# Kernel optimization log

Hardware: AMD Instinct MI355X
Metric: run time of the kernel (lower is better)

Reference implementation:

```python
import jax, jax.numpy as jnp
import numpy as np

B, S, E = 2, 2048, 1024
HID = 1024
HEADS = 16
EPS = 1e-5
SCALE = (E * 2) ** (-0.5)  # source uses input_data_dim*2


def setup_inputs() -> dict:
    key = jax.random.key(0)
    k1, k2, k3 = jax.random.split(key, 3)
    return {
        "x": jax.random.normal(k1, (B, S, E), dtype=jnp.float32),
        "ln_g": jnp.ones((E,), jnp.float32),
        "ln_b": jnp.zeros((E,), jnp.float32),
        "W1": jax.random.normal(k2, (E, 3 * HID), jnp.float32) * 0.02,
        "b1": jnp.zeros((3 * HID,), jnp.float32),
        "W2": jax.random.normal(k3, (HID, HID), jnp.float32) * 0.02,
        "b2": jnp.zeros((HID,), jnp.float32),
    }


def reference(x, ln_g, ln_b, W1, b1, W2, b2):
    # LayerNorm over last dim
    mu = jnp.mean(x, axis=-1, keepdims=True)
    var = jnp.mean(jnp.square(x - mu), axis=-1, keepdims=True)
    xn = (x - mu) * jax.lax.rsqrt(var + EPS) * ln_g + ln_b
    # QKV projection: [B,S,3*HID]
    qkv = jnp.einsum('bse,ef->bsf', xn, W1) + b1
    # Faithful to source: flat reshape to (heads, B, S, 3*HID/heads)
    qkv_heads = qkv.reshape(HEADS, B, S, -1)
    q, k, v = jnp.split(qkv_heads, 3, axis=-1)  # each [H,B,S,d]
    scores = jnp.einsum('hbse,hbSe->hbsS', q, k) * SCALE  # [H,B,S,S]
    att = jax.nn.softmax(scores, axis=-1)
    full_att = jnp.einsum('hbsS,hbSe->hbse', att, v)  # [H,B,S,d]
    full_att = full_att.reshape(B, S, -1)  # faithful flat reshape -> [B,S,HID]
    out = jnp.einsum('bsh,hk->bsk', full_att, W2) + b2
    return out
```

## Files before the change

### kernel.cpp

```cpp
#include <hip/hip_runtime.h>

typedef unsigned short u16;
typedef __bf16 bf16x8 __attribute__((ext_vector_type(8)));
typedef float f32x4 __attribute__((ext_vector_type(4)));

static constexpr float SCALE2 = 0.022097086912079608f * 1.4426950408889634f;

__device__ __forceinline__ u16 f2b(float f) {
  union { float f; unsigned int i; } v; v.f = f;
  unsigned int r = v.i + 0x7fffu + ((v.i >> 16) & 1u);
  return (u16)(r >> 16);
}
__device__ __forceinline__ unsigned int pk2(float a, float b) {
#if __has_builtin(__builtin_amdgcn_cvt_pk_bf16_f32)
  auto v = __builtin_amdgcn_cvt_pk_bf16_f32(a, b);
  unsigned int u;
  __builtin_memcpy(&u, &v, 4);
  return u;
#else
  union { float f; unsigned int i; } x, y; x.f = a; y.f = b;
  return ((x.i + 0x8000u) >> 16) | ((y.i + 0x8000u) & 0xffff0000u);
#endif
}
__device__ __forceinline__ void async16(const u16* g, u16* l) {
  __builtin_amdgcn_global_load_lds((const __attribute__((address_space(1))) void*)g,
                                   (__attribute__((address_space(3))) void*)l,
                                   16, 0, 0);
}

__global__ __launch_bounds__(256) void pre_kernel(const float* __restrict__ x,
                                                  const float* __restrict__ lg,
                                                  const float* __restrict__ lb,
                                                  u16* __restrict__ xn,
                                                  const float* __restrict__ W1,
                                                  u16* __restrict__ W1T,
                                                  const float* __restrict__ W2,
                                                  u16* __restrict__ W2T) {
  __shared__ __align__(16) u16 smem[64 * 72];
  const int bx = blockIdx.x;
  const int t = threadIdx.x;
  if (bx < 4096) {
    float* red = (float*)smem;
    const int row = bx;
    float4 v = *(const float4*)(x + (size_t)row * 1024 + t * 4);
    float s = v.x + v.y + v.z + v.w;
    float ss = v.x * v.x + v.y * v.y + v.z * v.z + v.w * v.w;
    for (int off = 32; off >= 1; off >>= 1) {
      s += __shfl_xor(s, off, 64);
      ss += __shfl_xor(ss, off, 64);
    }
    const int w = t >> 6;
    if ((t & 63) == 0) { red[w] = s; red[4 + w] = ss; }
    __syncthreads();
    s = red[0] + red[1] + red[2] + red[3];
    ss = red[4] + red[5] + red[6] + red[7];
    const float mu = s * (1.0f / 1024.0f);
    const float var = ss * (1.0f / 1024.0f) - mu * mu;
    const float inv = rsqrtf(var + 1e-5f);
    float4 gg = *(const float4*)(lg + t * 4);
    float4 bb = *(const float4*)(lb + t * 4);
    ushort4 o;
    o.x = f2b((v.x - mu) * inv * gg.x + bb.x);
    o.y = f2b((v.y - mu) * inv * gg.y + bb.y);
    o.z = f2b((v.z - mu) * inv * gg.z + bb.z);
    o.w = f2b((v.w - mu) * inv * gg.w + bb.w);
    *(ushort4*)(xn + (size_t)row * 1024 + t * 4) = o;
    return;
  }
  const float* in;
  u16* out;
  int C, c0, r0;
  if (bx < 4096 + 768) {
    const int idx = bx - 4096;
    C = 3072; in = W1; out = W1T;
    c0 = (idx % 48) * 64; r0 = (idx / 48) * 64;
  } else {
    const int idx = bx - 4864;
    C = 1024; in = W2; out = W2T;
    c0 = (idx % 16) * 64; r0 = (idx / 16) * 64;
  }
  const int row = t >> 2, cseg = t & 3;
  for (int it = 0; it < 4; it++) {
    float4 v = *(const float4*)&in[(size_t)(r0 + row) * C + c0 + it * 16 + cseg * 4];
    ushort4 o;
    o.x = f2b(v.x); o.y = f2b(v.y); o.z = f2b(v.z); o.w = f2b(v.w);
    *(ushort4*)&smem[row * 72 + it * 16 + cseg * 4] = o;
  }
  __syncthreads();
  const int orow = t >> 2, ch = t & 3;
  u16 vals[16];
  for (int j = 0; j < 16; j++) vals[j] = smem[(ch * 16 + j) * 72 + orow];
  u16* dp = out + (size_t)(c0 + orow) * 1024 + r0 + ch * 16;
  *(uint4*)&dp[0] = *(uint4*)&vals[0];
  *(uint4*)&dp[8] = *(uint4*)&vals[8];
}

template <int MODE, int MT>
__global__ __launch_bounds__(256) void gemm_bt(const u16* __restrict__ A,
                                               const u16* __restrict__ Bt,
                                               const float* __restrict__ bias,
                                               float* __restrict__ C,
                                               int M, int N, int K,
                                               u16* __restrict__ Qc,
                                               u16* __restrict__ Kc,
                                               u16* __restrict__ Vtmp) {
  __shared__ __align__(16) u16 SMEM[8192];
  u16* As = SMEM;
  u16* Bs = SMEM + MT * 32;
  const int m0 = blockIdx.y * MT, n0 = blockIdx.x * 128;
  const int t = threadIdx.x, w = t >> 6, lane = t & 63;
  const int q = lane >> 4, l16 = lane & 15;
  const int wm = (w >> 1) * (MT / 2), wn = (w & 1) * 64;
  constexpr int NI = MT / 32;

  const int sc = (lane & 3) ^ ((lane >> 3) & 3);
  const u16* ap = A + (size_t)(m0 + w * 16 + (lane >> 2)) * K + sc * 8;
  const u16* bp = Bt + (size_t)(n0 + w * 16 + (lane >> 2)) * K + sc * 8;
  u16* lA = &As[w * 512];
  u16* lB = &Bs[w * 512];
  const int ac = q ^ ((l16 >> 1) & 3);

  f32x4 acc[NI][4];
  const f32x4 zero = {0.f, 0.f, 0.f, 0.f};
  for (int i = 0; i < NI; i++)
    for (int j = 0; j < 4; j++) acc[i][j] = zero;

  for (int k0 = 0; k0 < K; k0 += 32) {
    for (int i = 0; i < MT / 64; i++)
      async16(ap + (size_t)(i * 64) * K, lA + i * 2048);
    for (int i = 0; i < 2; i++)
      async16(bp + (size_t)(i * 64) * K, lB + i * 2048);
    ap += 32; bp += 32;
    __syncthreads();
    bf16x8 af[NI], bfr[4];
    for (int i = 0; i < NI; i++)
      af[i] = *(const bf16x8*)&As[(wm + i * 16 + l16) * 32 + ac * 8];
    for (int j = 0; j < 4; j++)
      bfr[j] = *(const bf16x8*)&Bs[(wn + j * 16 + l16) * 32 + ac * 8];
    for (int i = 0; i < NI; i++)
      for (int j = 0; j < 4; j++)
        acc[i][j] = __builtin_amdgcn_mfma_f32_16x16x32_bf16(af[i], bfr[j], acc[i][j], 0, 0, 0);
    __syncthreads();
  }

  if constexpr (MODE == 0) {
    for (int j = 0; j < 4; j++) {
      const int col = n0 + wn + j * 16 + l16;
      const float bv = bias[col];
      for (int i = 0; i < NI; i++) {
        const int rbase = m0 + wm + i * 16 + q * 4;
        for (int r = 0; r < 4; r++)
          C[(size_t)(rbase + r) * N + col] = acc[i][j][r] + bv;
      }
    }
  } else {
    const int seg = n0 + wn;
    const int k64 = seg >> 6;
    const int tcol = k64 / 3;
    const int typ = k64 - tcol * 3;
    u16* dst = (typ == 0) ? Qc : (typ == 1) ? Kc : Vtmp;
    const float qs = (typ == 0) ? SCALE2 : 1.0f;
    const int gidx = m0 >> 7;
    u16* tw = &SMEM[w * 1280];
    float bv[4];
    for (int j = 0; j < 4; j++) bv[j] = bias[seg + j * 16 + l16];
    __syncthreads();
    for (int i = 0; i < 4; i++) {
      for (int j = 0; j < 4; j++) {
        ushort4 pk;
        pk.x = f2b((acc[i][j][0] + bv[j]) * qs);
        pk.y = f2b((acc[i][j][1] + bv[j]) * qs);
        pk.z = f2b((acc[i][j][2] + bv[j]) * qs);
        pk.w = f2b((acc[i][j][3] + bv[j]) * qs);
        *(ushort4*)&tw[(j * 16 + l16) * 20 + q * 4] = pk;
      }
      const int r2 = lane >> 2;
      const int quarter = lane & 3;
      u16 vals[16];
      for (int c = 0; c < 16; c++)
        vals[c] = tw[(quarter * 16 + c) * 20 + r2];
      const int lr = wm + i * 16 + r2;
      const int s = (lr << 4) + tcol;
      u16* dp = dst + ((size_t)gidx * 2048 + s) * 64 + quarter * 16;
      *(uint4*)&dp[0] = *(uint4*)&vals[0];
      *(uint4*)&dp[8] = *(uint4*)&vals[8];
    }
  }
}

__global__ __launch_bounds__(256) void vtrans(const u16* __restrict__ Vtmp,
                                              u16* __restrict__ Vt) {
  __shared__ __align__(16) u16 tile[64 * 64];
  const int g = blockIdx.y, s0 = blockIdx.x * 64;
  const int t = threadIdx.x;
  const int row = t >> 3, ch = t & 7;
  for (int p = 0; p < 2; p++) {
    const int r = p * 32 + row;
    uint4 v = *(const uint4*)&Vtmp[((size_t)g * 2048 + s0 + r) * 64 + ch * 8];
    *(uint4*)&tile[r * 64 + ((ch ^ (r & 7)) * 8)] = v;
  }
  __syncthreads();
  const int d = t >> 2, scn = t & 3;
  u16 vals[16];
  for (int j2 = 0; j2 < 16; j2++) {
    const int s = scn * 16 + j2;
    vals[j2] = tile[s * 64 + (((d >> 3) ^ (s & 7)) * 8) + (d & 7)];
  }
  u16* dp = Vt + ((size_t)g * 64 + d) * 2048 + s0 + scn * 16;
  *(uint4*)&dp[0] = *(uint4*)&vals[0];
  *(uint4*)&dp[8] = *(uint4*)&vals[8];
}

__global__ __launch_bounds__(512) void attn_kernel(const u16* __restrict__ Qc,
                                                   const u16* __restrict__ Kc,
                                                   const u16* __restrict__ Vt,
                                                   u16* __restrict__ Oc) {
  __shared__ __align__(16) u16 LDS[25600];
  u16* K0 = LDS;
  u16* K1 = LDS + 4096;
  u16* V0 = LDS + 8192;
  u16* V1 = LDS + 12288;
  u16* Ps = LDS + 16384;
  const int g = blockIdx.y;
  const int q0 = blockIdx.x * 128;
  const int t = threadIdx.x, w = t >> 6, lane = t & 63;
  const int q = lane >> 4, l16 = lane & 15;

  const u16* Qg = Qc + (size_t)g * 2048 * 64;
  const u16* Kg = Kc + (size_t)g * 2048 * 64;
  const u16* Vg = Vt + (size_t)g * 64 * 2048;

  bf16x8 aq[2];
  for (int ks = 0; ks < 2; ks++)
    aq[ks] = *(const bf16x8*)&Qg[(size_t)(q0 + w * 16 + l16) * 64 + ks * 32 + q * 8];

  f32x4 accO[4];
  const f32x4 zero = {0.f, 0.f, 0.f, 0.f};
  for (int c = 0; c < 4; c++) accO[c] = zero;
  f32x4 psv = zero;

  const int ch = (lane & 7) ^ ((lane >> 3) & 7);
  const u16* kp = Kg + (size_t)(w * 8 + (lane >> 3)) * 64 + ch * 8;
  const u16* vp = Vg + (size_t)(w * 8 + (lane >> 3)) * 2048 + ch * 8;
  u16* lK0 = K0 + w * 512;
  u16* lK1 = K1 + w * 512;
  u16* lV0 = V0 + w * 512;
  u16* lV1 = V1 + w * 512;

  const int kch = q ^ (l16 & 7);
  const int pb = w * 1152;

  async16(kp, lK0);
  async16(vp, lV0);
  __syncthreads();

  for (int it = 0; it < 32; it++) {
    const int cur = it & 1;
    const u16* Kcur = cur ? K1 : K0;
    const u16* Vcur = cur ? V1 : V0;
    if (it < 31) {
      const int kt0 = (it + 1) * 64;
      async16(kp + (size_t)kt0 * 64, cur ? lK0 : lK1);
      async16(vp + kt0, cur ? lV0 : lV1);
    }

    f32x4 sa[4];
    __builtin_amdgcn_s_setprio(1);
    for (int ct = 0; ct < 4; ct++) {
      bf16x8 bk0 = *(const bf16x8*)&Kcur[(ct * 16 + l16) * 64 + kch * 8];
      bf16x8 bk1 = *(const bf16x8*)&Kcur[(ct * 16 + l16) * 64 + (kch ^ 4) * 8];
      f32x4 a = zero;
      a = __builtin_amdgcn_mfma_f32_16x16x32_bf16(bk0, aq[0], a, 0, 0, 0);
      a = __builtin_amdgcn_mfma_f32_16x16x32_bf16(bk1, aq[1], a, 0, 0, 0);
      sa[ct] = a;
    }
    __builtin_amdgcn_s_setprio(0);

    {
      u16* Pr = &Ps[pb + l16 * 72];
      for (int ct = 0; ct < 4; ct++) {
        f32x4 p;
        for (int r = 0; r < 4; r++) p[r] = __builtin_amdgcn_exp2f(sa[ct][r]);
        psv += p;
        uint2 pk;
        pk.x = pk2(p[0], p[1]);
        pk.y = pk2(p[2], p[3]);
        *(uint2*)&Pr[ct * 16 + q * 4] = pk;
      }
    }

    __builtin_amdgcn_s_setprio(1);
    for (int k2 = 0; k2 < 2; k2++) {
      bf16x8 apf = *(const bf16x8*)&Ps[pb + l16 * 72 + k2 * 32 + q * 8];
      for (int c = 0; c < 4; c++) {
        const int vch = (k2 * 4 + q) ^ (l16 & 7);
        bf16x8 bv = *(const bf16x8*)&Vcur[(c * 16 + l16) * 64 + vch * 8];
        accO[c] = __builtin_amdgcn_mfma_f32_16x16x32_bf16(bv, apf, accO[c], 0, 0, 0);
      }
    }
    __builtin_amdgcn_s_setprio(0);

    __syncthreads();
  }

  {
    float lsum = psv[0] + psv[1] + psv[2] + psv[3];
    lsum += __shfl_xor(lsum, 16, 64);
    lsum += __shfl_xor(lsum, 32, 64);
    const int srow = q0 + w * 16 + l16;
    const int orow = g * 128 + (srow >> 4);
    const int cbase = (srow & 15) * 64;
    const float linv = 1.0f / lsum;
    for (int c = 0; c < 4; c++) {
      ushort4 o;
      o.x = f2b(accO[c][0] * linv);
      o.y = f2b(accO[c][1] * linv);
      o.z = f2b(accO[c][2] * linv);
      o.w = f2b(accO[c][3] * linv);
      *(ushort4*)&Oc[(size_t)orow * 1024 + cbase + c * 16 + q * 4] = o;
    }
  }
}

extern "C" void kernel_launch(void* const* d_in, const int* in_sizes, int n_in,
                              void* d_out, int out_size, void* d_ws, size_t ws_size,
                              hipStream_t stream) {
  (void)in_sizes; (void)n_in; (void)out_size; (void)ws_size;
  const float* x    = (const float*)d_in[0];
  const float* ln_g = (const float*)d_in[1];
  const float* ln_b = (const float*)d_in[2];
  const float* W1   = (const float*)d_in[3];
  const float* b1   = (const float*)d_in[4];
  const float* W2   = (const float*)d_in[5];
  const float* b2   = (const float*)d_in[6];

  char* ws = (char*)d_ws;
  u16* xn   = (u16*)(ws);
  u16* W1T  = (u16*)(ws + ((size_t)8 << 20));
  u16* W2T  = (u16*)(ws + ((size_t)14 << 20));
  u16* Qc   = (u16*)(ws + ((size_t)16 << 20));
  u16* Kc   = (u16*)(ws + ((size_t)24 << 20));
  u16* Vtmp = (u16*)(ws + ((size_t)32 << 20));
  u16* Vt   = (u16*)(ws + ((size_t)40 << 20));
  u16* Oc   = xn;

  pre_kernel<<<dim3(5120), dim3(256), 0, stream>>>(x, ln_g, ln_b, xn, W1, W1T, W2, W2T);
  gemm_bt<1, 128><<<dim3(24, 32), dim3(256), 0, stream>>>(xn, W1T, b1, nullptr,
                                                          4096, 3072, 1024, Qc, Kc, Vtmp);
  vtrans<<<dim3(32, 32), dim3(256), 0, stream>>>(Vtmp, Vt);
  attn_kernel<<<dim3(16, 32), dim3(512), 0, stream>>>(Qc, Kc, Vt, Oc);
  gemm_bt<0, 64><<<dim3(8, 64), dim3(256), 0, stream>>>(Oc, W2T, b2, (float*)d_out,
                                                        4096, 1024, 1024, nullptr, nullptr, nullptr);
}
```

Measured before the change: 196.3 us.

## Switch attention to 32x32 MFMA with register P via permlane swap and KV split

Rewrites the attention inner loop to use 32x32x16 bf16 MFMA instructions. Each wave now handles 32 query rows and half of each 64-key tile, so eight waves cover 128 queries by splitting the KV tile in two. The softmax probabilities are repacked into MFMA operand layout in registers with permlane32_swap instead of going through an LDS scratch buffer. A final LDS reduction merges the partial O accumulators and row sums of the two KV halves. This removes the LDS round trip for P and reduces the number of MFMA issues, at the cost of an epilogue reduction, more accumulator registers and a dependence on gfx950-specific permlane instructions.

```diff
diff --git a/kernel.cpp b/kernel.cpp
--- a/kernel.cpp
+++ b/kernel.cpp
@@ -3,6 +3,9 @@
 typedef unsigned short u16;
 typedef __bf16 bf16x8 __attribute__((ext_vector_type(8)));
 typedef float f32x4 __attribute__((ext_vector_type(4)));
+typedef float f32x16 __attribute__((ext_vector_type(16)));
+typedef unsigned int u32x4 __attribute__((ext_vector_type(4)));
+typedef int i32x2 __attribute__((ext_vector_type(2)));
 
 static constexpr float SCALE2 = 0.022097086912079608f * 1.4426950408889634f;
 
@@ -20,6 +23,15 @@
 #else
   union { float f; unsigned int i; } x, y; x.f = a; y.f = b;
   return ((x.i + 0x8000u) >> 16) | ((y.i + 0x8000u) & 0xffff0000u);
+#endif
+}
+__device__ __forceinline__ i32x2 plswap(unsigned int a, unsigned int b) {
+#if __has_builtin(__builtin_amdgcn_permlane32_swap)
+  return __builtin_amdgcn_permlane32_swap((int)a, (int)b, false, false);
+#else
+  int d = (int)a, s = (int)b;
+  asm volatile("v_permlane32_swap_b32 %0, %1" : "+v"(d), "+v"(s));
+  i32x2 r; r[0] = d; r[1] = s; return r;
 #endif
 }
 __device__ __forceinline__ void async16(const u16* g, u16* l) {
@@ -220,24 +232,28 @@
   u16* K1 = LDS + 4096;
   u16* V0 = LDS + 8192;
   u16* V1 = LDS + 12288;
-  u16* Ps = LDS + 16384;
   const int g = blockIdx.y;
   const int q0 = blockIdx.x * 128;
   const int t = threadIdx.x, w = t >> 6, lane = t & 63;
-  const int q = lane >> 4, l16 = lane & 15;
+  const int l31 = lane & 31, h = lane >> 5;
+  const int qs = w & 3;
+  const int kvb = (w >> 2) * 32;
 
   const u16* Qg = Qc + (size_t)g * 2048 * 64;
   const u16* Kg = Kc + (size_t)g * 2048 * 64;
   const u16* Vg = Vt + (size_t)g * 64 * 2048;
 
-  bf16x8 aq[2];
-  for (int ks = 0; ks < 2; ks++)
-    aq[ks] = *(const bf16x8*)&Qg[(size_t)(q0 + w * 16 + l16) * 64 + ks * 32 + q * 8];
-
-  f32x4 accO[4];
-  const f32x4 zero = {0.f, 0.f, 0.f, 0.f};
-  for (int c = 0; c < 4; c++) accO[c] = zero;
-  f32x4 psv = zero;
+  bf16x8 aq[4];
+#pragma unroll
+  for (int s = 0; s < 4; s++)
+    aq[s] = *(const bf16x8*)&Qg[(size_t)(q0 + qs * 32 + l31) * 64 + s * 16 + h * 8];
+
+  f32x16 accO[2];
+#pragma unroll
+  for (int tt = 0; tt < 2; tt++)
+#pragma unroll
+    for (int r = 0; r < 16; r++) accO[tt][r] = 0.f;
+  float psv = 0.f;
 
   const int ch = (lane & 7) ^ ((lane >> 3) & 7);
   const u16* kp = Kg + (size_t)(w * 8 + (lane >> 3)) * 64 + ch * 8;
@@ -247,8 +263,7 @@
   u16* lV0 = V0 + w * 512;
   u16* lV1 = V1 + w * 512;
 
-  const int kch = q ^ (l16 & 7);
-  const int pb = w * 1152;
+  const int rsw = l31 & 7;
 
   async16(kp, lK0);
   async16(vp, lV0);
@@ -264,38 +279,42 @@
       async16(vp + kt0, cur ? lV0 : lV1);
     }
 
-    f32x4 sa[4];
+    f32x16 sa;
+#pragma unroll
+    for (int r = 0; r < 16; r++) sa[r] = 0.f;
     __builtin_amdgcn_s_setprio(1);
-    for (int ct = 0; ct < 4; ct++) {
-      bf16x8 bk0 = *(const bf16x8*)&Kcur[(ct * 16 + l16) * 64 + kch * 8];
-      bf16x8 bk1 = *(const bf16x8*)&Kcur[(ct * 16 + l16) * 64 + (kch ^ 4) * 8];
-      f32x4 a = zero;
-      a = __builtin_amdgcn_mfma_f32_16x16x32_bf16(bk0, aq[0], a, 0, 0, 0);
-      a = __builtin_amdgcn_mfma_f32_16x16x32_bf16(bk1, aq[1], a, 0, 0, 0);
-      sa[ct] = a;
+#pragma unroll
+    for (int s = 0; s < 4; s++) {
+      bf16x8 ak = *(const bf16x8*)&Kcur[(kvb + l31) * 64 + (((s * 2 + h) ^ rsw) * 8)];
+      sa = __builtin_amdgcn_mfma_f32_32x32x16_bf16(ak, aq[s], sa, 0, 0, 0);
     }
     __builtin_amdgcn_s_setprio(0);
 
-    {
-      u16* Pr = &Ps[pb + l16 * 72];
-      for (int ct = 0; ct < 4; ct++) {
-        f32x4 p;
-        for (int r = 0; r < 4; r++) p[r] = __builtin_amdgcn_exp2f(sa[ct][r]);
-        psv += p;
-        uint2 pk;
-        pk.x = pk2(p[0], p[1]);
-        pk.y = pk2(p[2], p[3]);
-        *(uint2*)&Pr[ct * 16 + q * 4] = pk;
-      }
-    }
+    float e[16];
+#pragma unroll
+    for (int r = 0; r < 16; r++) e[r] = __builtin_amdgcn_exp2f(sa[r]);
+    psv += (((e[0] + e[1]) + (e[2] + e[3])) + ((e[4] + e[5]) + (e[6] + e[7])))
+         + (((e[8] + e[9]) + (e[10] + e[11])) + ((e[12] + e[13]) + (e[14] + e[15])));
+    unsigned int c[8];
+#pragma unroll
+    for (int m = 0; m < 8; m++) c[m] = pk2(e[2 * m], e[2 * m + 1]);
+    i32x2 r02 = plswap(c[0], c[2]);
+    i32x2 r13 = plswap(c[1], c[3]);
+    i32x2 r46 = plswap(c[4], c[6]);
+    i32x2 r57 = plswap(c[5], c[7]);
+    bf16x8 pf[2];
+    u32x4 f0 = {(unsigned)r02[0], (unsigned)r13[0], (unsigned)r02[1], (unsigned)r13[1]};
+    u32x4 f1 = {(unsigned)r46[0], (unsigned)r57[0], (unsigned)r46[1], (unsigned)r57[1]};
+    __builtin_memcpy(&pf[0], &f0, 16);
+    __builtin_memcpy(&pf[1], &f1, 16);
 
     __builtin_amdgcn_s_setprio(1);
-    for (int k2 = 0; k2 < 2; k2++) {
-      bf16x8 apf = *(const bf16x8*)&Ps[pb + l16 * 72 + k2 * 32 + q * 8];
-      for (int c = 0; c < 4; c++) {
-        const int vch = (k2 * 4 + q) ^ (l16 & 7);
-        bf16x8 bv = *(const bf16x8*)&Vcur[(c * 16 + l16) * 64 + vch * 8];
-        accO[c] = __builtin_amdgcn_mfma_f32_16x16x32_bf16(bv, apf, accO[c], 0, 0, 0);
+#pragma unroll
+    for (int s = 0; s < 2; s++) {
+#pragma unroll
+      for (int tt = 0; tt < 2; tt++) {
+        bf16x8 av = *(const bf16x8*)&Vcur[(tt * 32 + l31) * 64 + ((((kvb >> 3) + s * 2 + h) ^ rsw) * 8)];
+        accO[tt] = __builtin_amdgcn_mfma_f32_32x32x16_bf16(av, pf[s], accO[tt], 0, 0, 0);
       }
     }
     __builtin_amdgcn_s_setprio(0);
@@ -303,22 +322,47 @@
     __syncthreads();
   }
 
-  {
-    float lsum = psv[0] + psv[1] + psv[2] + psv[3];
-    lsum += __shfl_xor(lsum, 16, 64);
-    lsum += __shfl_xor(lsum, 32, 64);
-    const int srow = q0 + w * 16 + l16;
+  float* Red = (float*)LDS;
+  if (w >= 4) {
+    const int base = (w - 4) * 2048;
+#pragma unroll
+    for (int tt = 0; tt < 2; tt++)
+#pragma unroll
+      for (int m = 0; m < 4; m++) {
+        f32x4 v4 = {accO[tt][4 * m], accO[tt][4 * m + 1], accO[tt][4 * m + 2], accO[tt][4 * m + 3]};
+        *(f32x4*)&Red[base + (tt * 4 + m) * 256 + lane * 4] = v4;
+      }
+    Red[8192 + (w - 4) * 64 + lane] = psv;
+  }
+  __syncthreads();
+  if (w < 4) {
+#pragma unroll
+    for (int tt = 0; tt < 2; tt++)
+#pragma unroll
+      for (int m = 0; m < 4; m++) {
+        f32x4 v4 = *(const f32x4*)&Red[w * 2048 + (tt * 4 + m) * 256 + lane * 4];
+        accO[tt][4 * m + 0] += v4[0];
+        accO[tt][4 * m + 1] += v4[1];
+        accO[tt][4 * m + 2] += v4[2];
+        accO[tt][4 * m + 3] += v4[3];
+      }
+    psv += Red[8192 + w * 64 + lane];
+    psv += __shfl_xor(psv, 32, 64);
+    const float linv = 1.0f / psv;
+    const int srow = q0 + qs * 32 + l31;
     const int orow = g * 128 + (srow >> 4);
     const int cbase = (srow & 15) * 64;
-    const float linv = 1.0f / lsum;
-    for (int c = 0; c < 4; c++) {
-      ushort4 o;
-      o.x = f2b(accO[c][0] * linv);
-      o.y = f2b(accO[c][1] * linv);
-      o.z = f2b(accO[c][2] * linv);
-      o.w = f2b(accO[c][3] * linv);
-      *(ushort4*)&Oc[(size_t)orow * 1024 + cbase + c * 16 + q * 4] = o;
-    }
+#pragma unroll
+    for (int tt = 0; tt < 2; tt++)
+#pragma unroll
+      for (int m = 0; m < 4; m++) {
+        ushort4 o;
+        o.x = f2b(accO[tt][4 * m + 0] * linv);
+        o.y = f2b(accO[tt][4 * m + 1] * linv);
+        o.z = f2b(accO[tt][4 * m + 2] * linv);
+        o.w = f2b(accO[tt][4 * m + 3] * linv);
+        *(ushort4*)&Oc[(size_t)orow * 1024 + cbase + tt * 32 + m * 8 + h * 4] = o;
+      }
   }
 }
 
```

New measurement: 195.2 us. No clear change (-0.6%).
